# Kernel tuning notes

Hardware: AMD Instinct MI355X
Metric: run time of the kernel (lower is better)

The kernel has to match this reference:

```python
import jax, jax.numpy as jnp
import numpy as np

B, S, D, H = 2, 2048, 1024, 16
HD = D // H  # head_dim = 64


def setup_inputs() -> dict:
    key = jax.random.key(0)
    ks = jax.random.split(key, 10)
    std = 1.0 / np.sqrt(D)
    inputs = jax.random.normal(ks[0], (B, S, D), dtype=jnp.float32)
    # stacked per-head projection weights: [H, HD, D] (row-major like nn.Linear)
    Wq = jax.random.uniform(ks[1], (H, HD, D), jnp.float32, -std, std)
    bq = jax.random.uniform(ks[2], (H, HD), jnp.float32, -std, std)
    Wk = jax.random.uniform(ks[3], (H, HD, D), jnp.float32, -std, std)
    bk = jax.random.uniform(ks[4], (H, HD), jnp.float32, -std, std)
    Wv = jax.random.uniform(ks[5], (H, HD, D), jnp.float32, -std, std)
    bv = jax.random.uniform(ks[6], (H, HD), jnp.float32, -std, std)
    Wo = jax.random.uniform(ks[7], (D, D), jnp.float32, -std, std)
    bo = jax.random.uniform(ks[8], (D,), jnp.float32, -std, std)
    return {"inputs": inputs, "Wq": Wq, "bq": bq, "Wk": Wk, "bk": bk,
            "Wv": Wv, "bv": bv, "Wo": Wo, "bo": bo}


def reference(inputs, Wq, bq, Wk, bk, Wv, bv, Wo, bo):
    # per-head projections, batched over heads: [B,H,S,HD]
    q = jnp.einsum('bsd,hed->bhse', inputs, Wq) + bq[None, :, None, :]
    k = jnp.einsum('bsd,hed->bhse', inputs, Wk) + bk[None, :, None, :]
    v = jnp.einsum('bsd,hed->bhse', inputs, Wv) + bv[None, :, None, :]
    scale = 1.0 / np.sqrt(HD).astype(np.float32)
    # explicit [B,H,S,S] score matrix, as in the original naive attention
    scores = jnp.einsum('bhqe,bhke->bhqk', q, k) * scale
    causal = jnp.tril(jnp.ones((S, S), dtype=bool))
    scores = jnp.where(causal[None, None], scores, jnp.float32(-jnp.inf))
    attn = jax.nn.softmax(scores, axis=-1)  # dropout p=0 -> identity
    wv = jnp.einsum('bhqk,bhke->bhqe', attn, v)
    # concat heads along feature dim: [B,S,H*HD] = [B,S,D]
    z = wv.transpose(0, 2, 1, 3).reshape(B, S, D)
    out = jnp.einsum('bsd,ed->bse', z, Wo) + bo
    return out
```

## Files before the change

kernel.cpp:

```cpp
#include <hip/hip_runtime.h>
#include <math.h>

#define Bx 2
#define Sx 2048
#define Dx 1024
#define Hx 16
#define HDx 64
#define Mx (Bx*Sx)

typedef __bf16 bf16x8 __attribute__((ext_vector_type(8)));
typedef __bf16 bf16x4 __attribute__((ext_vector_type(4)));
typedef float  f32x4  __attribute__((ext_vector_type(4)));

#define SCL 0.18033688011112042f

__device__ __forceinline__ void gload_lds16(const __bf16* g, __bf16* l) {
  __builtin_amdgcn_global_load_lds(
      (const __attribute__((address_space(1))) unsigned int*)g,
      (__attribute__((address_space(3))) unsigned int*)l, 16, 0, 0);
}

__device__ __forceinline__ void cvt8(const float* s, __bf16* d) {
  float4 a = *(const float4*)s;
  float4 b = *(const float4*)(s + 4);
  bf16x8 o;
  o[0] = (__bf16)a.x; o[1] = (__bf16)a.y; o[2] = (__bf16)a.z; o[3] = (__bf16)a.w;
  o[4] = (__bf16)b.x; o[5] = (__bf16)b.y; o[6] = (__bf16)b.z; o[7] = (__bf16)b.w;
  *(bf16x8*)d = o;
}

__global__ __launch_bounds__(256) void cvt_kernel(
    const float* __restrict__ x, const float* __restrict__ Wq,
    const float* __restrict__ Wk, const float* __restrict__ Wv,
    const float* __restrict__ Wo, const float* __restrict__ bq,
    const float* __restrict__ bk, const float* __restrict__ bv,
    __bf16* __restrict__ xb, __bf16* __restrict__ wqkv,
    __bf16* __restrict__ wob, float* __restrict__ bqkv)
{
  const int bid = blockIdx.x;
  const int t = threadIdx.x;
  const size_t MEG = 1024u * 1024u;
  if (bid < 2048) {
    size_t e = (size_t)bid * 2048 + t * 8;
    cvt8(x + e, xb + e);
  } else if (bid < 3584) {
    size_t e = (size_t)(bid - 2048) * 2048 + t * 8;
    const float* src = (e < MEG) ? (Wq + e) : (e < 2 * MEG) ? (Wk + (e - MEG)) : (Wv + (e - 2 * MEG));
    cvt8(src, wqkv + e);
  } else if (bid < 4096) {
    size_t e = (size_t)(bid - 3584) * 2048 + t * 8;
    cvt8(Wo + e, wob + e);
  } else {
    for (int i = t; i < 3072; i += 256)
      bqkv[i] = (i < 1024) ? bq[i] : (i < 2048) ? bk[i - 1024] : bv[i - 2048];
  }
}

template<int TM, int TN, int MODE>
__global__ __launch_bounds__(256) void gemm_k(
    const __bf16* __restrict__ A, const __bf16* __restrict__ W,
    const float* __restrict__ bias, float* __restrict__ Cf,
    __bf16* __restrict__ Cb, __bf16* __restrict__ vT,
    int M, int N, int K, int ldc)
{
  constexpr int MS = TM / 32;
  constexpr int NS = TN / 32;
  __shared__ __bf16 As[TM * 32];
  __shared__ __bf16 Bs[TN * 32];
  const int tid = threadIdx.x;
  const int lane = tid & 63, wave = tid >> 6;
  const int l16 = lane & 15, quad = lane >> 4;
  const int wm = (wave >> 1) * (TM / 2);
  const int wn = (wave & 1) * (TN / 2);
  const int m0 = blockIdx.y * TM;
  const int n0 = blockIdx.x * TN;

  const f32x4 zero = {0.f, 0.f, 0.f, 0.f};
  f32x4 acc[MS][NS];
#pragma unroll
  for (int i = 0; i < MS; ++i)
#pragma unroll
    for (int j = 0; j < NS; ++j) acc[i][j] = zero;

  const int arow = tid >> 2;
  const int achk = (tid & 3) * 8;
  const __bf16* Ag = A + (size_t)(m0 + arow) * K + achk;
  const __bf16* Wg = W + (size_t)(n0 + arow) * K + achk;

  for (int k0 = 0; k0 < K; k0 += 32) {
    __syncthreads();
#pragma unroll
    for (int i = 0; i < TM / 64; ++i)
      gload_lds16(Ag + (size_t)i * 64 * K + k0, &As[(i * 256 + tid) * 8]);
#pragma unroll
    for (int i = 0; i < TN / 64; ++i)
      gload_lds16(Wg + (size_t)i * 64 * K + k0, &Bs[(i * 256 + tid) * 8]);
    __syncthreads();

    bf16x8 af[MS], bfr[NS];
#pragma unroll
    for (int i = 0; i < MS; ++i)
      af[i] = *(const bf16x8*)&As[(wm + i * 16 + l16) * 32 + quad * 8];
#pragma unroll
    for (int j = 0; j < NS; ++j)
      bfr[j] = *(const bf16x8*)&Bs[(wn + j * 16 + l16) * 32 + quad * 8];
#pragma unroll
    for (int i = 0; i < MS; ++i)
#pragma unroll
      for (int j = 0; j < NS; ++j)
        acc[i][j] = __builtin_amdgcn_mfma_f32_16x16x32_bf16(af[i], bfr[j], acc[i][j], 0, 0, 0);
  }

  const int cbase = n0 + wn + l16;
#pragma unroll
  for (int j = 0; j < NS; ++j) {
    const int c = cbase + j * 16;
    const float bv_ = bias[c];
#pragma unroll
    for (int i = 0; i < MS; ++i) {
      const int r0 = m0 + wm + i * 16 + quad * 4;
      if (MODE == 0) {
#pragma unroll
        for (int g = 0; g < 4; ++g)
          Cf[(size_t)(r0 + g) * ldc + c] = acc[i][j][g] + bv_;
      } else {
        if (c < 2048) {
          const float sc = (c < 1024) ? SCL : 1.0f;
#pragma unroll
          for (int g = 0; g < 4; ++g)
            Cb[(size_t)(r0 + g) * 3072 + c] = (__bf16)((acc[i][j][g] + bv_) * sc);
        } else {
          const int c2 = c - 2048;
          const int hh = c2 >> 6, dd = c2 & 63;
          const int bb = r0 >> 11, ss = r0 & 2047;
          bf16x4 st;
          st[0] = (__bf16)(acc[i][j][0] + bv_);
          st[1] = (__bf16)(acc[i][j][1] + bv_);
          st[2] = (__bf16)(acc[i][j][2] + bv_);
          st[3] = (__bf16)(acc[i][j][3] + bv_);
          *(bf16x4*)&vT[((size_t)(bb * 16 + hh) * 64 + dd) * 2048 + ss] = st;
        }
      }
    }
  }
}

__global__ __launch_bounds__(256) void attn_mfma(
    const __bf16* __restrict__ qkv, const __bf16* __restrict__ vT,
    __bf16* __restrict__ zb)
{
  __shared__ __bf16 Qs[64 * 64];
  __shared__ __bf16 Ks[2][64 * 64];
  __shared__ __bf16 Vs[2][64 * 64];

  const int tid = threadIdx.x;
  const int lane = tid & 63, wave = tid >> 6;
  const int l16 = lane & 15, quad = lane >> 4;
  const int bx = blockIdx.x;
  const int qt = 31 - (bx >> 5);
  const int bh = bx & 31;
  const int h = bh & 15, b = bh >> 4;
  const int q0 = qt * 64;

  const __bf16* qg = qkv + (size_t)b * 2048 * 3072 + h * 64;
  const __bf16* kg = qg + 1024;
  const __bf16* vg = vT + (size_t)bh * 64 * 2048;

#pragma unroll
  for (int i = 0; i < 2; ++i) {
    int slot = i * 256 + tid;
    int row = slot >> 3, ph = slot & 7;
    int cs = ph ^ (row & 7);
    gload_lds16(qg + (size_t)(q0 + row) * 3072 + cs * 8, &Qs[slot * 8]);
    gload_lds16(kg + (size_t)row * 3072 + cs * 8, &Ks[0][slot * 8]);
    gload_lds16(vg + (size_t)row * 2048 + cs * 8, &Vs[0][slot * 8]);
  }
  __syncthreads();

  const int sw0 = ((quad) ^ (l16 & 7)) * 8;
  const int sw1 = ((quad + 4) ^ (l16 & 7)) * 8;
  const int mrow = wave * 16 + l16;

  bf16x8 qf0 = *(const bf16x8*)&Qs[mrow * 64 + sw0];
  bf16x8 qf1 = *(const bf16x8*)&Qs[mrow * 64 + sw1];
  __bf16* P = &Qs[wave * 16 * 64];

  bf16x8 onesf;
  {
    __bf16 ov = (l16 == 0) ? (__bf16)1.0f : (__bf16)0.0f;
#pragma unroll
    for (int i = 0; i < 8; ++i) onesf[i] = ov;
  }

  const f32x4 zero = {0.f, 0.f, 0.f, 0.f};
  f32x4 O[4], Ol = zero;
#pragma unroll
  for (int j = 0; j < 4; ++j) O[j] = zero;

  const int rq = q0 + wave * 16 + quad * 4;

#define ATTN_TILE(bb, DIAG)                                                     \
  {                                                                             \
    f32x4 s_[4];                                                                \
    _Pragma("unroll")                                                           \
    for (int j = 0; j < 4; ++j) s_[j] = zero;                                   \
    _Pragma("unroll")                                                           \
    for (int j = 0; j < 4; ++j) {                                               \
      bf16x8 kf0 = *(const bf16x8*)&Ks[bb][(j * 16 + l16) * 64 + sw0];          \
      s_[j] = __builtin_amdgcn_mfma_f32_16x16x32_bf16(qf0, kf0, s_[j], 0, 0, 0);\
      bf16x8 kf1 = *(const bf16x8*)&Ks[bb][(j * 16 + l16) * 64 + sw1];          \
      s_[j] = __builtin_amdgcn_mfma_f32_16x16x32_bf16(qf1, kf1, s_[j], 0, 0, 0);\
    }                                                                           \
    _Pragma("unroll")                                                           \
    for (int j = 0; j < 4; ++j) {                                               \
      _Pragma("unroll")                                                         \
      for (int g = 0; g < 4; ++g) {                                             \
        float p = __builtin_exp2f(s_[j][g]);                                    \
        if (DIAG && (j * 16 + l16) > (wave * 16 + quad * 4 + g)) p = 0.f;       \
        s_[j][g] = p;                                                           \
      }                                                                         \
    }                                                                           \
    _Pragma("unroll")                                                           \
    for (int j = 0; j < 4; ++j) {                                               \
      const int col = j * 16 + l16;                                             \
      const int ch = col >> 3, cin = col & 7;                                   \
      _Pragma("unroll")                                                         \
      for (int g = 0; g < 4; ++g) {                                             \
        const int row = quad * 4 + g;                                           \
        P[row * 64 + ((ch ^ (row & 7)) * 8) + cin] = (__bf16)s_[j][g];          \
      }                                                                         \
    }                                                                           \
    {                                                                           \
      bf16x8 pf0 = *(const bf16x8*)&P[l16 * 64 + sw0];                          \
      bf16x8 pf1 = *(const bf16x8*)&P[l16 * 64 + sw1];                          \
      _Pragma("unroll")                                                         \
      for (int j = 0; j < 4; ++j) {                                             \
        bf16x8 vf0 = *(const bf16x8*)&Vs[bb][(j * 16 + l16) * 64 + sw0];        \
        O[j] = __builtin_amdgcn_mfma_f32_16x16x32_bf16(pf0, vf0, O[j], 0, 0, 0);\
        bf16x8 vf1 = *(const bf16x8*)&Vs[bb][(j * 16 + l16) * 64 + sw1];        \
        O[j] = __builtin_amdgcn_mfma_f32_16x16x32_bf16(pf1, vf1, O[j], 0, 0, 0);\
      }                                                                         \
      Ol = __builtin_amdgcn_mfma_f32_16x16x32_bf16(pf0, onesf, Ol, 0, 0, 0);    \
      Ol = __builtin_amdgcn_mfma_f32_16x16x32_bf16(pf1, onesf, Ol, 0, 0, 0);    \
    }                                                                           \
  }

  for (int kt = 0; kt < qt; ++kt) {
    const int bb = kt & 1;
    const int kn = (kt + 1) * 64;
    const int nb = bb ^ 1;
#pragma unroll
    for (int i = 0; i < 2; ++i) {
      int slot = i * 256 + tid;
      int row = slot >> 3, ph = slot & 7;
      int cs = ph ^ (row & 7);
      gload_lds16(kg + (size_t)(kn + row) * 3072 + cs * 8, &Ks[nb][slot * 8]);
      gload_lds16(vg + (size_t)row * 2048 + kn + cs * 8, &Vs[nb][slot * 8]);
    }
    ATTN_TILE(bb, false)
    __syncthreads();
  }
  ATTN_TILE((qt & 1), true)

#pragma unroll
  for (int g = 0; g < 4; ++g) {
    const float lv = __shfl(Ol[g], lane & 48);
    const float inv = 1.0f / lv;
    const size_t rb = (size_t)(b * 2048 + rq + g) * 1024 + h * 64 + l16;
#pragma unroll
    for (int j = 0; j < 4; ++j)
      zb[rb + j * 16] = (__bf16)(O[j][g] * inv);
  }
}

extern "C" void kernel_launch(void* const* d_in, const int* in_sizes, int n_in,
                              void* d_out, int out_size, void* d_ws, size_t ws_size,
                              hipStream_t stream) {
  (void)in_sizes; (void)n_in; (void)out_size; (void)ws_size;
  const float* x  = (const float*)d_in[0];
  const float* Wq = (const float*)d_in[1];
  const float* bq = (const float*)d_in[2];
  const float* Wk = (const float*)d_in[3];
  const float* bk = (const float*)d_in[4];
  const float* Wv = (const float*)d_in[5];
  const float* bv = (const float*)d_in[6];
  const float* Wo = (const float*)d_in[7];
  const float* bo = (const float*)d_in[8];

  char* ws = (char*)d_ws;
  __bf16* xb   = (__bf16*)(ws);
  __bf16* wqkv = (__bf16*)(ws + (8ull  << 20));
  __bf16* wob  = (__bf16*)(ws + (14ull << 20));
  float*  bqkv = (float*) (ws + (16ull << 20));
  __bf16* qkv  = (__bf16*)(ws + (17ull << 20));
  __bf16* vT   = (__bf16*)(ws + (41ull << 20));
  __bf16* zb   = (__bf16*)(ws + (49ull << 20));

  cvt_kernel<<<4097, 256, 0, stream>>>(x, Wq, Wk, Wv, Wo, bq, bk, bv,
                                       xb, wqkv, wob, bqkv);
  gemm_k<128, 128, 1><<<dim3(24, 32), 256, 0, stream>>>(
      xb, wqkv, bqkv, nullptr, qkv, vT, Mx, 3072, 1024, 0);
  attn_mfma<<<1024, 256, 0, stream>>>(qkv, vT, zb);
  gemm_k<128, 64, 0><<<dim3(16, 32), 256, 0, stream>>>(
      zb, wob, bo, (float*)d_out, nullptr, nullptr, Mx, 1024, 1024, 1024);
}
```

Before: 198.3 us.

## Deepen GEMM K-tile with swizzled LDS and software-pipeline attention S/PV

The GEMM kernel now stages 64-wide K slices per iteration using an XOR-swizzled LDS layout, which halves the number of barrier pairs and is meant to avoid bank conflicts. The attention kernel is restructured into a software pipeline. The QK^T score tile for the next key block is computed while the current block's softmax and PV products run, with a triple-buffered V and a prefetch issued two tiles ahead. This adds LDS and register pressure (the extra score accumulators), which may lower occupancy.

```diff
diff --git a/kernel.cpp b/kernel.cpp
--- a/kernel.cpp
+++ b/kernel.cpp
@@ -65,8 +65,8 @@
 {
   constexpr int MS = TM / 32;
   constexpr int NS = TN / 32;
-  __shared__ __bf16 As[TM * 32];
-  __shared__ __bf16 Bs[TN * 32];
+  __shared__ __bf16 As[TM * 64];
+  __shared__ __bf16 Bs[TN * 64];
   const int tid = threadIdx.x;
   const int lane = tid & 63, wave = tid >> 6;
   const int l16 = lane & 15, quad = lane >> 4;
@@ -74,6 +74,7 @@
   const int wn = (wave & 1) * (TN / 2);
   const int m0 = blockIdx.y * TM;
   const int n0 = blockIdx.x * TN;
+  const int swz = l16 & 7;
 
   const f32x4 zero = {0.f, 0.f, 0.f, 0.f};
   f32x4 acc[MS][NS];
@@ -82,33 +83,37 @@
 #pragma unroll
     for (int j = 0; j < NS; ++j) acc[i][j] = zero;
 
-  const int arow = tid >> 2;
-  const int achk = (tid & 3) * 8;
-  const __bf16* Ag = A + (size_t)(m0 + arow) * K + achk;
-  const __bf16* Wg = W + (size_t)(n0 + arow) * K + achk;
-
-  for (int k0 = 0; k0 < K; k0 += 32) {
+  const int srow = tid >> 3;
+  const int scs = (tid & 7) ^ (srow & 7);
+  const __bf16* Ag = A + (size_t)(m0 + srow) * K + scs * 8;
+  const __bf16* Wg = W + (size_t)(n0 + srow) * K + scs * 8;
+
+  for (int k0 = 0; k0 < K; k0 += 64) {
     __syncthreads();
 #pragma unroll
-    for (int i = 0; i < TM / 64; ++i)
-      gload_lds16(Ag + (size_t)i * 64 * K + k0, &As[(i * 256 + tid) * 8]);
-#pragma unroll
-    for (int i = 0; i < TN / 64; ++i)
-      gload_lds16(Wg + (size_t)i * 64 * K + k0, &Bs[(i * 256 + tid) * 8]);
+    for (int i = 0; i < TM / 32; ++i)
+      gload_lds16(Ag + (size_t)(i * 32) * K + k0, &As[(i * 256 + tid) * 8]);
+#pragma unroll
+    for (int i = 0; i < TN / 32; ++i)
+      gload_lds16(Wg + (size_t)(i * 32) * K + k0, &Bs[(i * 256 + tid) * 8]);
     __syncthreads();
 
-    bf16x8 af[MS], bfr[NS];
-#pragma unroll
-    for (int i = 0; i < MS; ++i)
-      af[i] = *(const bf16x8*)&As[(wm + i * 16 + l16) * 32 + quad * 8];
-#pragma unroll
-    for (int j = 0; j < NS; ++j)
-      bfr[j] = *(const bf16x8*)&Bs[(wn + j * 16 + l16) * 32 + quad * 8];
-#pragma unroll
-    for (int i = 0; i < MS; ++i)
+#pragma unroll
+    for (int hk = 0; hk < 2; ++hk) {
+      const int ph = ((hk * 4 + quad) ^ swz) * 8;
+      bf16x8 af[MS], bfr[NS];
+#pragma unroll
+      for (int i = 0; i < MS; ++i)
+        af[i] = *(const bf16x8*)&As[(wm + i * 16 + l16) * 64 + ph];
 #pragma unroll
       for (int j = 0; j < NS; ++j)
-        acc[i][j] = __builtin_amdgcn_mfma_f32_16x16x32_bf16(af[i], bfr[j], acc[i][j], 0, 0, 0);
+        bfr[j] = *(const bf16x8*)&Bs[(wn + j * 16 + l16) * 64 + ph];
+#pragma unroll
+      for (int i = 0; i < MS; ++i)
+#pragma unroll
+        for (int j = 0; j < NS; ++j)
+          acc[i][j] = __builtin_amdgcn_mfma_f32_16x16x32_bf16(af[i], bfr[j], acc[i][j], 0, 0, 0);
+    }
   }
 
   const int cbase = n0 + wn + l16;
@@ -151,7 +156,7 @@
 {
   __shared__ __bf16 Qs[64 * 64];
   __shared__ __bf16 Ks[2][64 * 64];
-  __shared__ __bf16 Vs[2][64 * 64];
+  __shared__ __bf16 Vs[3][64 * 64];
 
   const int tid = threadIdx.x;
   const int lane = tid & 63, wave = tid >> 6;
@@ -166,15 +171,25 @@
   const __bf16* kg = qg + 1024;
   const __bf16* vg = vT + (size_t)bh * 64 * 2048;
 
+#define STAGE_KV(kt_, kbuf, vbuf)                                               \
+  { const int kn = (kt_) * 64;                                                  \
+    _Pragma("unroll")                                                           \
+    for (int i = 0; i < 2; ++i) {                                               \
+      int slot = i * 256 + tid;                                                 \
+      int row = slot >> 3, ph2 = slot & 7;                                      \
+      int cs = ph2 ^ (row & 7);                                                 \
+      gload_lds16(kg + (size_t)(kn + row) * 3072 + cs * 8, &Ks[kbuf][slot * 8]);\
+      gload_lds16(vg + (size_t)row * 2048 + kn + cs * 8, &Vs[vbuf][slot * 8]);  \
+    } }
+
 #pragma unroll
   for (int i = 0; i < 2; ++i) {
     int slot = i * 256 + tid;
-    int row = slot >> 3, ph = slot & 7;
-    int cs = ph ^ (row & 7);
+    int row = slot >> 3, ph2 = slot & 7;
+    int cs = ph2 ^ (row & 7);
     gload_lds16(qg + (size_t)(q0 + row) * 3072 + cs * 8, &Qs[slot * 8]);
-    gload_lds16(kg + (size_t)row * 3072 + cs * 8, &Ks[0][slot * 8]);
-    gload_lds16(vg + (size_t)row * 2048 + cs * 8, &Vs[0][slot * 8]);
-  }
+  }
+  STAGE_KV(0, 0, 0)
   __syncthreads();
 
   const int sw0 = ((quad) ^ (l16 & 7)) * 8;
@@ -196,28 +211,27 @@
   f32x4 O[4], Ol = zero;
 #pragma unroll
   for (int j = 0; j < 4; ++j) O[j] = zero;
-
-  const int rq = q0 + wave * 16 + quad * 4;
-
-#define ATTN_TILE(bb, DIAG)                                                     \
-  {                                                                             \
-    f32x4 s_[4];                                                                \
-    _Pragma("unroll")                                                           \
-    for (int j = 0; j < 4; ++j) s_[j] = zero;                                   \
+  f32x4 s_cur[4], s_next[4];
+
+#define S_TILE(sdst, kb)                                                        \
+  { _Pragma("unroll")                                                           \
+    for (int j = 0; j < 4; ++j) sdst[j] = zero;                                 \
     _Pragma("unroll")                                                           \
     for (int j = 0; j < 4; ++j) {                                               \
-      bf16x8 kf0 = *(const bf16x8*)&Ks[bb][(j * 16 + l16) * 64 + sw0];          \
-      s_[j] = __builtin_amdgcn_mfma_f32_16x16x32_bf16(qf0, kf0, s_[j], 0, 0, 0);\
-      bf16x8 kf1 = *(const bf16x8*)&Ks[bb][(j * 16 + l16) * 64 + sw1];          \
-      s_[j] = __builtin_amdgcn_mfma_f32_16x16x32_bf16(qf1, kf1, s_[j], 0, 0, 0);\
-    }                                                                           \
-    _Pragma("unroll")                                                           \
+      bf16x8 kf0 = *(const bf16x8*)&Ks[kb][(j * 16 + l16) * 64 + sw0];          \
+      sdst[j] = __builtin_amdgcn_mfma_f32_16x16x32_bf16(qf0, kf0, sdst[j],0,0,0);\
+      bf16x8 kf1 = *(const bf16x8*)&Ks[kb][(j * 16 + l16) * 64 + sw1];          \
+      sdst[j] = __builtin_amdgcn_mfma_f32_16x16x32_bf16(qf1, kf1, sdst[j],0,0,0);\
+    } }
+
+#define EXP_P(s, DIAG)                                                          \
+  { _Pragma("unroll")                                                           \
     for (int j = 0; j < 4; ++j) {                                               \
       _Pragma("unroll")                                                         \
       for (int g = 0; g < 4; ++g) {                                             \
-        float p = __builtin_exp2f(s_[j][g]);                                    \
+        float p = __builtin_exp2f(s[j][g]);                                     \
         if (DIAG && (j * 16 + l16) > (wave * 16 + quad * 4 + g)) p = 0.f;       \
-        s_[j][g] = p;                                                           \
+        s[j][g] = p;                                                            \
       }                                                                         \
     }                                                                           \
     _Pragma("unroll")                                                           \
@@ -227,44 +241,43 @@
       _Pragma("unroll")                                                         \
       for (int g = 0; g < 4; ++g) {                                             \
         const int row = quad * 4 + g;                                           \
-        P[row * 64 + ((ch ^ (row & 7)) * 8) + cin] = (__bf16)s_[j][g];          \
+        P[row * 64 + ((ch ^ (row & 7)) * 8) + cin] = (__bf16)s[j][g];           \
       }                                                                         \
+    } }
+
+#define PV_TILE(vb)                                                             \
+  { bf16x8 pf0 = *(const bf16x8*)&P[l16 * 64 + sw0];                            \
+    bf16x8 pf1 = *(const bf16x8*)&P[l16 * 64 + sw1];                            \
+    _Pragma("unroll")                                                           \
+    for (int j = 0; j < 4; ++j) {                                               \
+      bf16x8 vf0 = *(const bf16x8*)&Vs[vb][(j * 16 + l16) * 64 + sw0];          \
+      O[j] = __builtin_amdgcn_mfma_f32_16x16x32_bf16(pf0, vf0, O[j], 0, 0, 0);  \
+      bf16x8 vf1 = *(const bf16x8*)&Vs[vb][(j * 16 + l16) * 64 + sw1];          \
+      O[j] = __builtin_amdgcn_mfma_f32_16x16x32_bf16(pf1, vf1, O[j], 0, 0, 0);  \
     }                                                                           \
-    {                                                                           \
-      bf16x8 pf0 = *(const bf16x8*)&P[l16 * 64 + sw0];                          \
-      bf16x8 pf1 = *(const bf16x8*)&P[l16 * 64 + sw1];                          \
-      _Pragma("unroll")                                                         \
-      for (int j = 0; j < 4; ++j) {                                             \
-        bf16x8 vf0 = *(const bf16x8*)&Vs[bb][(j * 16 + l16) * 64 + sw0];        \
-        O[j] = __builtin_amdgcn_mfma_f32_16x16x32_bf16(pf0, vf0, O[j], 0, 0, 0);\
-        bf16x8 vf1 = *(const bf16x8*)&Vs[bb][(j * 16 + l16) * 64 + sw1];        \
-        O[j] = __builtin_amdgcn_mfma_f32_16x16x32_bf16(pf1, vf1, O[j], 0, 0, 0);\
-      }                                                                         \
-      Ol = __builtin_amdgcn_mfma_f32_16x16x32_bf16(pf0, onesf, Ol, 0, 0, 0);    \
-      Ol = __builtin_amdgcn_mfma_f32_16x16x32_bf16(pf1, onesf, Ol, 0, 0, 0);    \
-    }                                                                           \
-  }
-
-  for (int kt = 0; kt < qt; ++kt) {
-    const int bb = kt & 1;
-    const int kn = (kt + 1) * 64;
-    const int nb = bb ^ 1;
-#pragma unroll
-    for (int i = 0; i < 2; ++i) {
-      int slot = i * 256 + tid;
-      int row = slot >> 3, ph = slot & 7;
-      int cs = ph ^ (row & 7);
-      gload_lds16(kg + (size_t)(kn + row) * 3072 + cs * 8, &Ks[nb][slot * 8]);
-      gload_lds16(vg + (size_t)row * 2048 + kn + cs * 8, &Vs[nb][slot * 8]);
-    }
-    ATTN_TILE(bb, false)
+    Ol = __builtin_amdgcn_mfma_f32_16x16x32_bf16(pf0, onesf, Ol, 0, 0, 0);      \
+    Ol = __builtin_amdgcn_mfma_f32_16x16x32_bf16(pf1, onesf, Ol, 0, 0, 0); }
+
+  if (qt > 0) STAGE_KV(1, 1, 1)
+  S_TILE(s_cur, 0)
+  if (qt > 0) __syncthreads();
+
+  for (int t = 0; t < qt; ++t) {
+    EXP_P(s_cur, false)
+    S_TILE(s_next, (t + 1) & 1)
+    PV_TILE(t % 3)
+    if (t + 2 <= qt) STAGE_KV(t + 2, t & 1, (t + 2) % 3)
     __syncthreads();
-  }
-  ATTN_TILE((qt & 1), true)
-
+#pragma unroll
+    for (int j = 0; j < 4; ++j) s_cur[j] = s_next[j];
+  }
+  EXP_P(s_cur, true)
+  PV_TILE(qt % 3)
+
+  const int rq = q0 + wave * 16 + quad * 4;
 #pragma unroll
   for (int g = 0; g < 4; ++g) {
-    const float lv = __shfl(Ol[g], lane & 48);
+    const float lv = __shfl(Ol[g], quad * 16);
     const float inv = 1.0f / lv;
     const size_t rb = (size_t)(b * 2048 + rq + g) * 1024 + h * 64 + l16;
 #pragma unroll
```

Measured after the change: 196.3 us. No clear change (-1.0%).
